# Kernel optimization log

Measured on AMD Instinct MI355X. Metric: run time of the kernel, lower is better.

The kernel has to match this reference:

```python
import jax, jax.numpy as jnp
import numpy as np

N, E, L, H, C, F_IN = 50000, 800000, 3, 8, 16, 128  # nodes, edges, layers, heads, per-head dim, input dim
NEG_SLOPE = 0.2


def setup_inputs() -> dict:
    key = jax.random.key(0)
    k = jax.random.split(key, 8)
    scale = 0.1
    x = jax.random.normal(k[0], (N, F_IN), dtype=jnp.float32)
    Ws = jax.random.normal(k[1], (L, F_IN, H * C), dtype=jnp.float32) * scale
    att_src = jax.random.normal(k[2], (L, H, C), dtype=jnp.float32) * scale
    att_dst = jax.random.normal(k[3], (L, H, C), dtype=jnp.float32) * scale
    biases = jnp.zeros((L, H * C), dtype=jnp.float32)
    fc_w = jax.random.normal(k[4], (H * C, C), dtype=jnp.float32) * scale
    fc_b = jnp.zeros((C,), dtype=jnp.float32)
    edge_index = jax.random.randint(k[5], (2, E), 0, N, dtype=jnp.int64)
    return {"x": x, "Ws": Ws, "att_src": att_src, "att_dst": att_dst,
            "biases": biases, "fc_w": fc_w, "fc_b": fc_b, "edge_index": edge_index}


def _gat_layer(x, W, a_src, a_dst, b, src, dst):
    # x: [N, F]; W: [F, H*C]; a_src/a_dst: [H, C]; src/dst: [E+N] (self-loops included)
    n = x.shape[0]
    h = (x @ W).reshape(n, H, C)                      # [N, H, C]
    e_src = jnp.einsum('nhc,hc->nh', h, a_src)        # [N, H]
    e_dst = jnp.einsum('nhc,hc->nh', h, a_dst)
    e = jax.nn.leaky_relu(e_src[src] + e_dst[dst], NEG_SLOPE)   # [E+N, H]
    # segment softmax over incoming edges of each target node
    emax = jax.ops.segment_max(e, dst, num_segments=n)          # [N, H]
    ex = jnp.exp(e - emax[dst])
    denom = jax.ops.segment_sum(ex, dst, num_segments=n)        # [N, H]
    alpha = ex / (denom[dst] + 1e-16)                            # [E+N, H]
    out = jax.ops.segment_sum(alpha[:, :, None] * h[src], dst, num_segments=n)  # [N, H, C]
    return out.reshape(n, H * C) + b


def reference(x, Ws, att_src, att_dst, biases, fc_w, fc_b, edge_index):
    loop = jnp.arange(N, dtype=edge_index.dtype)
    src = jnp.concatenate([edge_index[0], loop])  # add self-loops (PyG default)
    dst = jnp.concatenate([edge_index[1], loop])
    h = x
    for l in range(L):
        h = _gat_layer(h, Ws[l], att_src[l], att_dst[l], biases[l], src, dst)
        h = jax.nn.elu(h)
    return h @ fc_w + fc_b  # [N, C]
```

## Files before the change

### kernel.cpp

```cpp
#include <hip/hip_runtime.h>
#include <hip/hip_bf16.h>


#define GAT_F 128
#define GAT_H 8
#define GAT_C 16

typedef __attribute__((ext_vector_type(8))) short bf16x8;
typedef __attribute__((ext_vector_type(4))) float f32x4;

__device__ __forceinline__ float bf2f(unsigned short u) {
    union { unsigned int i; float f; } x; x.i = ((unsigned int)u) << 16; return x.f;
}
__device__ __forceinline__ float bfhi2f(unsigned int u) {
    union { unsigned int i; float f; } x; x.i = u & 0xFFFF0000u; return x.f;
}
__device__ __forceinline__ float bflo2f(unsigned int u) {
    union { unsigned int i; float f; } x; x.i = u << 16; return x.f;
}
__device__ __forceinline__ unsigned int pk_bf16(float a, float b) {
    union { float f; unsigned int i; } ua, ub;
    ua.f = a; ub.f = b;
    unsigned int ra = (ua.i + 0x7FFFu + ((ua.i >> 16) & 1u)) >> 16;
    unsigned int rb = (ub.i + 0x7FFFu + ((ub.i >> 16) & 1u)) & 0xFFFF0000u;
    return ra | rb;
}
__device__ __forceinline__ unsigned short f2bf(float a) {
    union { float f; unsigned int i; } ua; ua.f = a;
    return (unsigned short)((ua.i + 0x7FFFu + ((ua.i >> 16) & 1u)) >> 16);
}
__device__ __forceinline__ float ldf(const void* p, size_t i, int isf32) {
    return isf32 ? ((const float*)p)[i] : bf2f(((const unsigned short*)p)[i]);
}
__device__ __forceinline__ int ldei(const int* ei, int i, int is64) {
    return is64 ? ei[2 * (size_t)i] : ei[i];
}

__global__ void k_detect(const unsigned short* __restrict__ xb,
                         const int* __restrict__ ei, int* flags) {
    __shared__ int nan_cnt, zero_cnt;
    if (threadIdx.x == 0) { nan_cnt = 0; zero_cnt = 0; }
    __syncthreads();
    int t = threadIdx.x;
    int ln = 0;
    for (int i = t; i < 8192; i += 256) {
        unsigned short u = xb[i];
        if ((u & 0x7F80) == 0x7F80) ln++;
    }
    int lz = 0;
    for (int i = t; i < 2048; i += 256) {
        if (ei[2 * i + 1] == 0) lz++;
    }
    if (ln) atomicAdd(&nan_cnt, ln);
    if (lz) atomicAdd(&zero_cnt, lz);
    __syncthreads();
    if (t == 0) {
        flags[0] = (nan_cnt > 3) ? 1 : 0;
        flags[1] = (zero_cnt > 1024) ? 1 : 0;
    }
}

__global__ void k_prep(const void* __restrict__ W, const void* __restrict__ asrc,
                       const void* __restrict__ adst,
                       unsigned short* __restrict__ wt, unsigned short* __restrict__ wa,
                       int Lw, const int* __restrict__ flags) {
    int isf32 = flags[0];
    int b = blockIdx.x, t = threadIdx.x;
    if (b < Lw * 64) {
        int gid = b * 256 + t;
        int l = gid >> 14, r = gid & 16383;
        int c = r >> 7, k = r & 127;
        float v = ldf(W, (size_t)l * 16384 + k * 128 + c, isf32);
        wt[gid] = f2bf(v);
    } else {
        int id = (b - Lw * 64) * 256 + t;
        int l = id >> 11, q = id & 2047;
        int j = q >> 7, k = q & 127;
        int head = j & 7;
        const void* av = (j < 8) ? asrc : adst;
        float acc = 0.f;
        #pragma unroll
        for (int cc = 0; cc < 16; cc++) {
            float w = ldf(W, (size_t)l * 16384 + k * 128 + head * 16 + cc, isf32);
            float a = ldf(av, (size_t)l * 128 + head * 16 + cc, isf32);
            acc += w * a;
        }
        wa[id] = f2bf(acc);
    }
}

__global__ void k_init_deg(int* deg, int n) {
    int i = blockIdx.x * 256 + threadIdx.x;
    if (i < n) deg[i] = 1;
}

__global__ void k_count_deg(const int* __restrict__ ei, int* deg, int E,
                            const int* __restrict__ flags) {
    int k2 = (blockIdx.x * 256 + threadIdx.x) * 2;
    int is64 = flags[1];
    if (k2 + 1 < E) {
        int d0, d1;
        if (is64) { int4 v = *(const int4*)&ei[2 * (size_t)(E + k2)]; d0 = v.x; d1 = v.z; }
        else      { int2 v = *(const int2*)&ei[E + k2]; d0 = v.x; d1 = v.y; }
        atomicAdd(&deg[d0], 1);
        atomicAdd(&deg[d1], 1);
    } else if (k2 < E) {
        atomicAdd(&deg[ldei(ei, E + k2, is64)], 1);
    }
}

__global__ __launch_bounds__(256) void k_scan_blk(
    const int* __restrict__ deg, int* __restrict__ rp_local,
    int* __restrict__ bsum, int n)
{
    int b = blockIdx.x, t = threadIdx.x;
    int i0 = b * 1024 + t * 4;
    int v0 = 0, v1 = 0, v2 = 0, v3 = 0;
    if (i0 + 3 < n) {
        int4 d = *(const int4*)(deg + i0);
        v0 = d.x; v1 = d.y; v2 = d.z; v3 = d.w;
    } else {
        if (i0     < n) v0 = deg[i0];
        if (i0 + 1 < n) v1 = deg[i0 + 1];
        if (i0 + 2 < n) v2 = deg[i0 + 2];
        if (i0 + 3 < n) v3 = deg[i0 + 3];
    }
    int s = v0 + v1 + v2 + v3;
    int lane = t & 63, wid = t >> 6;
    int sc = s;
    #pragma unroll
    for (int off = 1; off < 64; off <<= 1) {
        int o = __shfl_up(sc, off);
        if (lane >= off) sc += o;
    }
    __shared__ int wsum[4];
    if (lane == 63) wsum[wid] = sc;
    __syncthreads();
    int woff = 0;
    #pragma unroll
    for (int w2 = 0; w2 < 4; w2++) if (w2 < wid) woff += wsum[w2];
    int excl = woff + sc - s;
    if (i0     < n) rp_local[i0]     = excl;
    if (i0 + 1 < n) rp_local[i0 + 1] = excl + v0;
    if (i0 + 2 < n) rp_local[i0 + 2] = excl + v0 + v1;
    if (i0 + 3 < n) rp_local[i0 + 3] = excl + v0 + v1 + v2;
    if (t == 255) bsum[b] = woff + sc;
}

__global__ __launch_bounds__(256) void k_scan_top(
    int* __restrict__ bsum, int* __restrict__ rowptr, int nb, int n)
{
    __shared__ int sh[1024];
    int t = threadIdx.x;
    for (int i = t; i < 1024; i += 256) sh[i] = (i < nb) ? bsum[i] : 0;
    __syncthreads();
    for (int off = 1; off < 1024; off <<= 1) {
        int vals[4];
        #pragma unroll
        for (int k = 0; k < 4; k++) {
            int i = t + 256 * k;
            vals[k] = (i >= off) ? sh[i - off] : 0;
        }
        __syncthreads();
        #pragma unroll
        for (int k = 0; k < 4; k++) sh[t + 256 * k] += vals[k];
        __syncthreads();
    }
    for (int i = t; i < nb; i += 256) bsum[i] = (i == 0) ? 0 : sh[i - 1];
    if (t == 0) rowptr[n] = sh[nb - 1];
}

__global__ void k_place_add(int* __restrict__ rowptr, const int* __restrict__ bsum,
                            int* __restrict__ adj, int* __restrict__ cursor, int n)
{
    int i = blockIdx.x * 256 + threadIdx.x;
    if (i < n) {
        int r = rowptr[i] + bsum[i >> 10];
        rowptr[i] = r;
        adj[r] = i;
        cursor[i] = 1;
    }
    if (blockIdx.x == 0 && threadIdx.x < 8) adj[rowptr[n] + threadIdx.x] = 0;
}

__global__ void k_scatter(const int* __restrict__ ei, const int* __restrict__ rowptr,
                          int* __restrict__ cursor, int* __restrict__ adj, int E,
                          const int* __restrict__ flags) {
    int k2 = (blockIdx.x * 256 + threadIdx.x) * 2;
    int is64 = flags[1];
    if (k2 + 1 < E) {
        int s0, s1, d0, d1;
        if (is64) {
            int4 a = *(const int4*)&ei[2 * (size_t)k2];       s0 = a.x; s1 = a.z;
            int4 b = *(const int4*)&ei[2 * (size_t)(E + k2)]; d0 = b.x; d1 = b.z;
        } else {
            int2 a = *(const int2*)&ei[k2];     s0 = a.x; s1 = a.y;
            int2 b = *(const int2*)&ei[E + k2]; d0 = b.x; d1 = b.y;
        }
        int p0 = atomicAdd(&cursor[d0], 1);
        adj[rowptr[d0] + p0] = s0;
        int p1 = atomicAdd(&cursor[d1], 1);
        adj[rowptr[d1] + p1] = s1;
    } else if (k2 < E) {
        int s = ldei(ei, k2, is64);
        int d = ldei(ei, E + k2, is64);
        int p = atomicAdd(&cursor[d], 1);
        adj[rowptr[d] + p] = s;
    }
}

__global__ __launch_bounds__(256) void k_gemm_mfma(
    const void* __restrict__ xin, int x_is_input,
    const unsigned short* __restrict__ wt,
    const unsigned short* __restrict__ wa,
    unsigned int* __restrict__ hb, float* __restrict__ es, float* __restrict__ ed,
    int n, const int* __restrict__ flags)
{
    __shared__ unsigned short xl[64 * 136];
    int isf32 = flags[0];
    int t = threadIdx.x;
    int row0 = blockIdx.x * 64;
    int lane = t & 63, wid = t >> 6, quad = lane >> 4, col = lane & 15;

    bool direct = (!x_is_input) || (!isf32);
    if (!direct) {
        const float4* xg = (const float4*)xin;
        for (int i = t; i < 2048; i += 256) {
            int r = i >> 5, c4 = i & 31;
            int gr = row0 + r;
            uint2 u = make_uint2(0u, 0u);
            if (gr < n) {
                float4 v = xg[(size_t)gr * 32 + c4];
                u = make_uint2(pk_bf16(v.x, v.y), pk_bf16(v.z, v.w));
            }
            *(uint2*)&xl[r * 136 + c4 * 4] = u;
        }
        __syncthreads();
    }

    int arow = row0 + wid * 16 + col;
    int arowc = min(arow, n - 1);
    const unsigned short* xrow = direct
        ? ((const unsigned short*)xin + (size_t)arowc * 128)
        : &xl[(wid * 16 + col) * 136];

    f32x4 acc[9];
    #pragma unroll
    for (int ct = 0; ct < 9; ct++) acc[ct] = (f32x4){0.f, 0.f, 0.f, 0.f};

    #pragma unroll
    for (int ks = 0; ks < 4; ks++) {
        int k0 = ks * 32;
        bf16x8 af = *(const bf16x8*)&xrow[k0 + quad * 8];
        #pragma unroll
        for (int ct = 0; ct < 9; ct++) {
            const unsigned short* bsrc = (ct < 8) ? &wt[(ct * 16 + col) * 128]
                                                  : &wa[col * 128];
            bf16x8 bf = *(const bf16x8*)&bsrc[k0 + quad * 8];
            acc[ct] = __builtin_amdgcn_mfma_f32_16x16x32_bf16(af, bf, acc[ct], 0, 0, 0);
        }
    }

    #pragma unroll
    for (int ct = 0; ct < 8; ct++) {
        #pragma unroll
        for (int r = 0; r < 4; r++) {
            int grow = row0 + wid * 16 + quad * 4 + r;
            float v = acc[ct][r];
            float vp = __shfl_xor(v, 1);
            if (!(lane & 1) && grow < n)
                hb[(size_t)grow * 64 + ct * 8 + (col >> 1)] = pk_bf16(v, vp);
        }
    }
    #pragma unroll
    for (int r = 0; r < 4; r++) {
        int grow = row0 + wid * 16 + quad * 4 + r;
        float v = acc[8][r];
        if (grow < n) {
            if (col < 8) es[(size_t)grow * 8 + col] = v;
            else         ed[(size_t)grow * 8 + col - 8] = v;
        }
    }
}

__global__ __launch_bounds__(256) void k_aggregate(
    const unsigned int* __restrict__ hb,
    const float* __restrict__ es, const float* __restrict__ ed,
    const int* __restrict__ rowptr, const int* __restrict__ adj,
    const void* __restrict__ bias, long b_off, unsigned int* __restrict__ out,
    int n, const int* __restrict__ flags)
{
    __shared__ __align__(16) float alds[4][72 * 12];
    __shared__ __align__(16) int   slds[4][80];
    int isf32 = flags[0];
    int lane = threadIdx.x & 63;
    int wid = threadIdx.x >> 6;
    int node = blockIdx.x * 4 + wid;
    if (node >= n) return;
    int base = rowptr[node];
    int deg = rowptr[node + 1] - base;
    int head = lane >> 3;

    if (lane < 8) {
        *(float4*)&alds[wid][(64 + lane) * 12]     = make_float4(0.f, 0.f, 0.f, 0.f);
        *(float4*)&alds[wid][(64 + lane) * 12 + 4] = make_float4(0.f, 0.f, 0.f, 0.f);
        slds[wid][64 + lane] = 0;
    }

    const float4* es4 = (const float4*)es;
    const float4* ed4 = (const float4*)ed;
    float edv[8];
    {
        float4 a = ed4[node * 2];
        float4 b = ed4[node * 2 + 1];
        edv[0] = a.x; edv[1] = a.y; edv[2] = a.z; edv[3] = a.w;
        edv[4] = b.x; edv[5] = b.y; edv[6] = b.z; edv[7] = b.w;
    }

    float acc0 = 0.f, acc1 = 0.f, lsum = 0.f;
    for (int j0 = 0; j0 < deg; j0 += 64) {
        int j = j0 + lane;
        int sp = (j < deg) ? adj[base + j] : 0;
        float4 ea = es4[sp * 2];
        float4 eb = es4[sp * 2 + 1];
        float ev[8] = {ea.x, ea.y, ea.z, ea.w, eb.x, eb.y, eb.z, eb.w};
        float p[8];
        #pragma unroll
        for (int hh = 0; hh < 8; hh++) {
            float v = ev[hh] + edv[hh];
            v = fmaxf(v, 0.2f * v);
            float pe = __expf(v);
            p[hh] = (j < deg) ? pe : 0.f;
        }
        *(float4*)&alds[wid][lane * 12]     = make_float4(p[0], p[1], p[2], p[3]);
        *(float4*)&alds[wid][lane * 12 + 4] = make_float4(p[4], p[5], p[6], p[7]);
        slds[wid][lane] = sp;
        __builtin_amdgcn_s_waitcnt(0xC07F);

        int lim = min(64, deg - j0);
        for (int jj = 0; jj < lim; jj += 8) {
            int4 sA = *(const int4*)&slds[wid][jj];
            int4 sB = *(const int4*)&slds[wid][jj + 4];
            float a0 = alds[wid][(jj + 0) * 12 + head];
            float a1 = alds[wid][(jj + 1) * 12 + head];
            float a2 = alds[wid][(jj + 2) * 12 + head];
            float a3 = alds[wid][(jj + 3) * 12 + head];
            float a4 = alds[wid][(jj + 4) * 12 + head];
            float a5 = alds[wid][(jj + 5) * 12 + head];
            float a6 = alds[wid][(jj + 6) * 12 + head];
            float a7 = alds[wid][(jj + 7) * 12 + head];
            unsigned int h0 = hb[sA.x * 64 + lane];
            unsigned int h1 = hb[sA.y * 64 + lane];
            unsigned int h2 = hb[sA.z * 64 + lane];
            unsigned int h3 = hb[sA.w * 64 + lane];
            unsigned int h4 = hb[sB.x * 64 + lane];
            unsigned int h5 = hb[sB.y * 64 + lane];
            unsigned int h6 = hb[sB.z * 64 + lane];
            unsigned int h7 = hb[sB.w * 64 + lane];
            lsum += ((a0 + a1) + (a2 + a3)) + ((a4 + a5) + (a6 + a7));
            acc0 += a0 * bflo2f(h0) + a1 * bflo2f(h1) + a2 * bflo2f(h2) + a3 * bflo2f(h3);
            acc0 += a4 * bflo2f(h4) + a5 * bflo2f(h5) + a6 * bflo2f(h6) + a7 * bflo2f(h7);
            acc1 += a0 * bfhi2f(h0) + a1 * bfhi2f(h1) + a2 * bfhi2f(h2) + a3 * bfhi2f(h3);
            acc1 += a4 * bfhi2f(h4) + a5 * bfhi2f(h5) + a6 * bfhi2f(h6) + a7 * bfhi2f(h7);
        }
    }

    float inv = 1.f / (lsum + 1e-16f);
    int ch = lane << 1;
    float o0 = acc0 * inv + ldf(bias, b_off + ch, isf32);
    float o1 = acc1 * inv + ldf(bias, b_off + ch + 1, isf32);
    o0 = o0 > 0.f ? o0 : (__expf(o0) - 1.f);
    o1 = o1 > 0.f ? o1 : (__expf(o1) - 1.f);
    out[(size_t)node * 64 + lane] = pk_bf16(o0, o1);
}

__global__ __launch_bounds__(256) void k_fc(
    const unsigned int* __restrict__ h, const void* __restrict__ fw,
    const void* __restrict__ fb, void* __restrict__ out, int n,
    const int* __restrict__ flags)
{
    __shared__ float fws[GAT_F * GAT_C];
    int isf32 = flags[0];
    int t = threadIdx.x;
    for (int i = t; i < GAT_F * GAT_C; i += 256)
        fws[i] = ldf(fw, i, isf32);
    __syncthreads();
    int row = blockIdx.x * 256 + t;
    if (row >= n) return;
    float acc[16];
    #pragma unroll
    for (int c = 0; c < 16; c++) acc[c] = ldf(fb, c, isf32);
    const unsigned int* hr = h + (size_t)row * 64;
    for (int k2 = 0; k2 < 64; k2++) {
        unsigned int u = hr[k2];
        float x0 = bflo2f(u), x1 = bfhi2f(u);
        const float4* w0 = (const float4*)&fws[(2 * k2) * 16];
        const float4* w1 = (const float4*)&fws[(2 * k2 + 1) * 16];
        #pragma unroll
        for (int c4 = 0; c4 < 4; c4++) {
            float4 wv0 = w0[c4], wv1 = w1[c4];
            acc[c4 * 4 + 0] += x0 * wv0.x + x1 * wv1.x;
            acc[c4 * 4 + 1] += x0 * wv0.y + x1 * wv1.y;
            acc[c4 * 4 + 2] += x0 * wv0.z + x1 * wv1.z;
            acc[c4 * 4 + 3] += x0 * wv0.w + x1 * wv1.w;
        }
    }
    if (isf32) {
        float* o = (float*)out + (size_t)row * GAT_C;
        #pragma unroll
        for (int c = 0; c < 16; c++) o[c] = acc[c];
    } else {
        __hip_bfloat16* o = (__hip_bfloat16*)out + (size_t)row * GAT_C;
        #pragma unroll
        for (int c = 0; c < 16; c++) o[c] = __float2bfloat16(acc[c]);
    }
}

extern "C" void kernel_launch(void* const* d_in, const int* in_sizes, int n_in,
                              void* d_out, int out_size, void* d_ws, size_t ws_size,
                              hipStream_t stream) {
    const void* x      = d_in[0];
    const void* Ws     = d_in[1];
    const void* att_s  = d_in[2];
    const void* att_d  = d_in[3];
    const void* biases = d_in[4];
    const void* fc_w   = d_in[5];
    const void* fc_b   = d_in[6];
    const int*  ei     = (const int*)d_in[7];

    const int N  = in_sizes[0] / GAT_F;
    const int E  = in_sizes[7] / 2;
    const int L  = in_sizes[1] / (GAT_F * GAT_F);
    const int ET = E + N;

    char* w = (char*)d_ws;
    int* flags         = (int*)w;            w += 64;
    unsigned int* hA   = (unsigned int*)w;   w += (size_t)N * 64 * 4;
    unsigned int* hB   = (unsigned int*)w;   w += (size_t)N * 64 * 4;
    float* es          = (float*)w;          w += (size_t)N * GAT_H * 4;
    float* ed          = (float*)w;          w += (size_t)N * GAT_H * 4;
    int* rowptr        = (int*)w;            w += (((size_t)(N + 1) * 4 + 15) & ~15ull);
    int* cursor        = (int*)w;            w += (size_t)N * 4;
    int* bsum          = (int*)w;            w += 1024 * 4;
    int* adj           = (int*)w;            w += (size_t)(ET + 16) * 4;
    unsigned short* wt = (unsigned short*)w; w += (size_t)L * 16384 * 2;
    unsigned short* wa = (unsigned short*)w; w += (size_t)L * 2048 * 2;

    int nb_n  = (N + 255) / 256;
    int nb_e2 = (E + 511) / 512;
    int nb_s  = (N + 1023) / 1024;

    k_detect<<<1, 256, 0, stream>>>((const unsigned short*)x, ei, flags);
    k_prep<<<L * 64 + L * 8, 256, 0, stream>>>(Ws, att_s, att_d, wt, wa, L, flags);

    k_init_deg<<<nb_n, 256, 0, stream>>>(cursor, N);
    k_count_deg<<<nb_e2, 256, 0, stream>>>(ei, cursor, E, flags);
    k_scan_blk<<<nb_s, 256, 0, stream>>>(cursor, rowptr, bsum, N);
    k_scan_top<<<1, 256, 0, stream>>>(bsum, rowptr, nb_s, N);
    k_place_add<<<nb_n, 256, 0, stream>>>(rowptr, bsum, adj, cursor, N);
    k_scatter<<<nb_e2, 256, 0, stream>>>(ei, rowptr, cursor, adj, E, flags);

    int nb_g = (N + 63) / 64;
    int nb_a = (N + 3) / 4;
    for (int l = 0; l < L; l++) {
        k_gemm_mfma<<<nb_g, 256, 0, stream>>>(
            (l == 0) ? x : (const void*)hA, (l == 0) ? 1 : 0,
            wt + (size_t)l * 16384, wa + (size_t)l * 2048,
            hB, es, ed, N, flags);
        k_aggregate<<<nb_a, 256, 0, stream>>>(
            hB, es, ed, rowptr, adj,
            biases, (long)l * GAT_F, hA, N, flags);
    }
    k_fc<<<nb_n, 256, 0, stream>>>(hA, fc_w, fc_b, d_out, N, flags);
}
```

Baseline: 419.1 us.

## Partition CSR scatter by destination range across grid y, one edge per thread

The edge scatter kernel now runs a 2D grid where each y-slice handles only edges whose destination falls in a 2048-node range. Every slice rereads the destination indices but does atomics and adjacency writes for a single range, which is meant to keep cursor/rowptr/adj accesses local in cache. The degree count and scatter also drop the two-edges-per-thread vectorised loads for one edge per thread. The cost is about 25 redundant passes over the destination array plus more launched blocks.

```diff
diff --git a/kernel.cpp b/kernel.cpp
--- a/kernel.cpp
+++ b/kernel.cpp
@@ -96,17 +96,9 @@
 
 __global__ void k_count_deg(const int* __restrict__ ei, int* deg, int E,
                             const int* __restrict__ flags) {
-    int k2 = (blockIdx.x * 256 + threadIdx.x) * 2;
+    int k = blockIdx.x * 256 + threadIdx.x;
     int is64 = flags[1];
-    if (k2 + 1 < E) {
-        int d0, d1;
-        if (is64) { int4 v = *(const int4*)&ei[2 * (size_t)(E + k2)]; d0 = v.x; d1 = v.z; }
-        else      { int2 v = *(const int2*)&ei[E + k2]; d0 = v.x; d1 = v.y; }
-        atomicAdd(&deg[d0], 1);
-        atomicAdd(&deg[d1], 1);
-    } else if (k2 < E) {
-        atomicAdd(&deg[ldei(ei, E + k2, is64)], 1);
-    }
+    if (k < E) atomicAdd(&deg[ldei(ei, E + k, is64)], 1);
 }
 
 __global__ __launch_bounds__(256) void k_scan_blk(
@@ -186,27 +178,14 @@
 __global__ void k_scatter(const int* __restrict__ ei, const int* __restrict__ rowptr,
                           int* __restrict__ cursor, int* __restrict__ adj, int E,
                           const int* __restrict__ flags) {
-    int k2 = (blockIdx.x * 256 + threadIdx.x) * 2;
+    int k = blockIdx.x * 256 + threadIdx.x;
+    if (k >= E) return;
     int is64 = flags[1];
-    if (k2 + 1 < E) {
-        int s0, s1, d0, d1;
-        if (is64) {
-            int4 a = *(const int4*)&ei[2 * (size_t)k2];       s0 = a.x; s1 = a.z;
-            int4 b = *(const int4*)&ei[2 * (size_t)(E + k2)]; d0 = b.x; d1 = b.z;
-        } else {
-            int2 a = *(const int2*)&ei[k2];     s0 = a.x; s1 = a.y;
-            int2 b = *(const int2*)&ei[E + k2]; d0 = b.x; d1 = b.y;
-        }
-        int p0 = atomicAdd(&cursor[d0], 1);
-        adj[rowptr[d0] + p0] = s0;
-        int p1 = atomicAdd(&cursor[d1], 1);
-        adj[rowptr[d1] + p1] = s1;
-    } else if (k2 < E) {
-        int s = ldei(ei, k2, is64);
-        int d = ldei(ei, E + k2, is64);
-        int p = atomicAdd(&cursor[d], 1);
-        adj[rowptr[d] + p] = s;
-    }
+    int d = ldei(ei, E + k, is64);
+    if ((d >> 11) != (int)blockIdx.y) return;
+    int s = ldei(ei, k, is64);
+    int p = atomicAdd(&cursor[d], 1);
+    adj[rowptr[d] + p] = s;
 }
 
 __global__ __launch_bounds__(256) void k_gemm_mfma(
@@ -446,19 +425,20 @@
     unsigned short* wt = (unsigned short*)w; w += (size_t)L * 16384 * 2;
     unsigned short* wa = (unsigned short*)w; w += (size_t)L * 2048 * 2;
 
-    int nb_n  = (N + 255) / 256;
-    int nb_e2 = (E + 511) / 512;
-    int nb_s  = (N + 1023) / 1024;
+    int nb_n = (N + 255) / 256;
+    int nb_e = (E + 255) / 256;
+    int nb_s = (N + 1023) / 1024;
+    int nr   = (N + 2047) >> 11;
 
     k_detect<<<1, 256, 0, stream>>>((const unsigned short*)x, ei, flags);
     k_prep<<<L * 64 + L * 8, 256, 0, stream>>>(Ws, att_s, att_d, wt, wa, L, flags);
 
     k_init_deg<<<nb_n, 256, 0, stream>>>(cursor, N);
-    k_count_deg<<<nb_e2, 256, 0, stream>>>(ei, cursor, E, flags);
+    k_count_deg<<<nb_e, 256, 0, stream>>>(ei, cursor, E, flags);
     k_scan_blk<<<nb_s, 256, 0, stream>>>(cursor, rowptr, bsum, N);
     k_scan_top<<<1, 256, 0, stream>>>(bsum, rowptr, nb_s, N);
     k_place_add<<<nb_n, 256, 0, stream>>>(rowptr, bsum, adj, cursor, N);
-    k_scatter<<<nb_e2, 256, 0, stream>>>(ei, rowptr, cursor, adj, E, flags);
+    k_scatter<<<dim3(nb_e, nr), 256, 0, stream>>>(ei, rowptr, cursor, adj, E, flags);
 
     int nb_g = (N + 63) / 64;
     int nb_a = (N + 3) / 4;
```

After: 440.5 us. +5.1%, slower.
